# Performance work log

Hardware: AMD Instinct MI355X
Metric: run time of the kernel (lower is better)

The kernel has to match this reference:

```python
import jax, jax.numpy as jnp
import numpy as np

E = 2048   # embedding_size
H = 2048   # hidden_size
B = 512    # batch
OUT = 2    # output_size (coords)


def setup_inputs() -> dict:
    key = jax.random.key(0)
    ks = jax.random.split(key, 11)
    s = 0.02
    return {
        "embedding": jax.random.normal(ks[0], (B, E), dtype=jnp.float32),
        "max_seq_length": 256,
        "W_embed": jax.random.normal(ks[1], (H, E), dtype=jnp.float32) * s,
        "b_embed": jnp.zeros((H,), dtype=jnp.float32),
        "W_ih": jax.random.normal(ks[2], (4 * H, OUT), dtype=jnp.float32) * s,
        "b_ih": jnp.zeros((4 * H,), dtype=jnp.float32),
        "W_hh": jax.random.normal(ks[3], (4 * H, H), dtype=jnp.float32) * s,
        "b_hh": jnp.zeros((4 * H,), dtype=jnp.float32),
        "W_out": jax.random.normal(ks[4], (OUT, H), dtype=jnp.float32) * s,
        "b_out": jnp.zeros((OUT,), dtype=jnp.float32),
        "W_stop": jax.random.normal(ks[5], (1, H), dtype=jnp.float32) * s,
        "b_stop": jnp.zeros((1,), dtype=jnp.float32),
    }


def reference(embedding, max_seq_length, W_embed, b_embed, W_ih, b_ih,
              W_hh, b_hh, W_out, b_out, W_stop, b_stop):
    # h_0 from embedding head (num_layers == 1)
    h0 = embedding @ W_embed.T + b_embed          # (B, H)
    c0 = jnp.zeros_like(h0)
    x0 = jnp.zeros((embedding.shape[0], OUT), dtype=embedding.dtype)

    def step(carry, _):
        h, c, x = carry
        gates = x @ W_ih.T + b_ih + h @ W_hh.T + b_hh    # (B, 4H)
        i, f, g, o = jnp.split(gates, 4, axis=-1)         # torch gate order i,f,g,o
        c = jax.nn.sigmoid(f) * c + jax.nn.sigmoid(i) * jnp.tanh(g)
        h = jax.nn.sigmoid(o) * jnp.tanh(c)
        coord = h @ W_out.T + b_out                        # (B, 2)
        stop = jax.nn.sigmoid(h @ W_stop.T + b_stop)       # (B, 1)
        return (h, c, coord), (coord, stop)

    _, (coords, stops) = jax.lax.scan(step, (h0, c0, x0), xs=None,
                                      length=max_seq_length)
    outputs = jnp.transpose(coords, (1, 0, 2))     # (B, T, 2)
    stop_probs = jnp.transpose(stops, (1, 0, 2))   # (B, T, 1)
    return outputs, stop_probs
```

## Files before the change

kernel.cpp:

```cpp
#include <hip/hip_runtime.h>
#include <stdint.h>

#define E_DIM 2048
#define H_DIM 2048
#define B_DIM 512
#define T_DIM 256
#define G4H   8192

typedef unsigned short u16;
typedef __attribute__((ext_vector_type(8))) short bf16x8;
typedef __attribute__((ext_vector_type(4))) float f32x4;

__device__ inline u16 f2b(float f) {
  union { float f; uint32_t i; } v; v.f = f;
  uint32_t u = v.i;
  return (u16)((u + 0x7FFFu + ((u >> 16) & 1u)) >> 16);
}
__device__ inline float b2f(u16 u) {
  union { uint32_t i; float f; } v; v.i = ((uint32_t)u) << 16; return v.f;
}

__global__ __launch_bounds__(256) void convert_bf16(const float* __restrict__ s,
                                                    u16* __restrict__ d, int n4) {
  int i = blockIdx.x * 256 + threadIdx.x;
  if (i < n4) {
    float4 f = ((const float4*)s)[i];
    ushort4 o;
    o.x = f2b(f.x); o.y = f2b(f.y); o.z = f2b(f.z); o.w = f2b(f.w);
    ((ushort4*)d)[i] = o;
  }
}

__global__ __launch_bounds__(256) void build_wswz(const float* __restrict__ W,
                                                  u16* __restrict__ Wz) {
  int id = blockIdx.x * 256 + threadIdx.x;
  int lane = id & 63;
  int k32  = (id >> 6) & 63;
  int n16  = id >> 12;
  int np = n16 * 16 + (lane & 15);
  int k  = k32 * 32 + (lane >> 4) * 8;
  int g = np & 3, jrow = np >> 2;
  const float* src = W + (size_t)(g * H_DIM + jrow) * H_DIM + k;
  float4 f0 = *(const float4*)(src);
  float4 f1 = *(const float4*)(src + 4);
  ushort4 o0, o1;
  o0.x = f2b(f0.x); o0.y = f2b(f0.y); o0.z = f2b(f0.z); o0.w = f2b(f0.w);
  o1.x = f2b(f1.x); o1.y = f2b(f1.y); o1.z = f2b(f1.z); o1.w = f2b(f1.w);
  u16* dst = Wz + (size_t)id * 8;
  *(ushort4*)(dst) = o0;
  *(ushort4*)(dst + 4) = o1;
}

__global__ __launch_bounds__(256) void build_epi(const float* __restrict__ b_ih,
                                                 const float* __restrict__ b_hh,
                                                 const float* __restrict__ W_ih,
                                                 float* __restrict__ epi) {
  int np = blockIdx.x * 256 + threadIdx.x;
  int src = (np & 3) * H_DIM + (np >> 2);
  float4 e;
  e.x = b_ih[src] + b_hh[src];
  e.y = W_ih[src * 2];
  e.z = W_ih[src * 2 + 1];
  e.w = 0.f;
  ((float4*)epi)[np] = e;
}

#define BM 64
#define BN 128
#define BK 32
__global__ __launch_bounds__(256) void gemm_bt(const u16* __restrict__ A,
                                               const u16* __restrict__ Bm,
                                               float* __restrict__ C,
                                               int M, int N, int K) {
  __shared__ u16 sA[BM * BK];
  __shared__ u16 sB[BN * BK];
  const int t = threadIdx.x;
  const int bm0 = blockIdx.y * BM, bn0 = blockIdx.x * BN;
  const int wave = t >> 6, lane = t & 63;
  const int wm = (wave >> 1) * 32, wn = (wave & 1) * 64;
  const int r16 = lane & 15, quad = lane >> 4;

  f32x4 acc[2][4];
  const f32x4 z = {0.f, 0.f, 0.f, 0.f};
  for (int i = 0; i < 2; ++i)
    for (int j = 0; j < 4; ++j) acc[i][j] = z;

  const int arow = t >> 2, acg = t & 3;

  for (int k0 = 0; k0 < K; k0 += BK) {
    __syncthreads();
    *(uint4*)&sA[arow * BK + acg * 8] =
        *(const uint4*)&A[(size_t)(bm0 + arow) * K + k0 + acg * 8];
    for (int i = 0; i < 2; ++i) {
      int c = t + 256 * i;
      int row = c >> 2, cg = c & 3;
      *(uint4*)&sB[row * BK + cg * 8] =
          *(const uint4*)&Bm[(size_t)(bn0 + row) * K + k0 + cg * 8];
    }
    __syncthreads();
    bf16x8 af[2], bfr[4];
    for (int mt = 0; mt < 2; ++mt)
      af[mt] = *(const bf16x8*)&sA[(wm + mt * 16 + r16) * BK + quad * 8];
    for (int nt = 0; nt < 4; ++nt)
      bfr[nt] = *(const bf16x8*)&sB[(wn + nt * 16 + r16) * BK + quad * 8];
    for (int mt = 0; mt < 2; ++mt)
      for (int nt = 0; nt < 4; ++nt)
        acc[mt][nt] = __builtin_amdgcn_mfma_f32_16x16x32_bf16(af[mt], bfr[nt],
                                                              acc[mt][nt], 0, 0, 0);
  }
  for (int mt = 0; mt < 2; ++mt)
    for (int nt = 0; nt < 4; ++nt) {
      int row = bm0 + wm + mt * 16 + quad * 4;
      int col = bn0 + wn + nt * 16 + r16;
      for (int r = 0; r < 4; ++r)
        C[(size_t)(row + r) * N + col] = acc[mt][nt][r];
    }
}

__global__ __launch_bounds__(256) void init_state(const float* __restrict__ h0pre,
                                                  const float* __restrict__ b_embed,
                                                  u16* __restrict__ h,
                                                  float* __restrict__ c,
                                                  float* __restrict__ x) {
  int idx = blockIdx.x * 256 + threadIdx.x;
  int bg = idx >> 11, k = idx & (H_DIM - 1);
  float v = h0pre[idx] + b_embed[k];
  size_t chunk = (((size_t)(bg >> 4)) * 64 + (k >> 5)) * 64 + ((k >> 3) & 3) * 16 + (bg & 15);
  size_t pos = chunk * 8 + (k & 7);
  h[pos] = f2b(v);
  c[pos] = 0.f;
  if (idx < B_DIM * 2) x[idx] = 0.f;
}

__global__ __launch_bounds__(512) void gemm_lstm(const u16* __restrict__ hA,
                                                 const u16* __restrict__ Wz,
                                                 const float* __restrict__ epi,
                                                 const float* __restrict__ x,
                                                 float* __restrict__ c,
                                                 u16* __restrict__ h_out) {
  __shared__ char smem[33792];
  float* gt   = (float*)smem;
  float* comb = (float*)smem;

  const int bid = blockIdx.x;
  const int nt = (bid & 7) * 8 + ((bid >> 3) & 7);
  const int mt = bid >> 6;
  const int bm0 = mt * 128;

  const int t = threadIdx.x, wv = t >> 6, ln = t & 63;
  const int q = wv & 3, kh = wv >> 2;
  const int qm = q & 1, qn = q >> 1;
  const int r16 = ln & 15, quad = ln >> 4;

  const u16* pA[4];
  const u16* pB[4];
  for (int i = 0; i < 4; ++i) {
    pA[i] = hA + (size_t)((bm0 >> 4) + qm * 4 + i) * 32768 +
            (size_t)(kh * 32) * 512 + ln * 8;
    pB[i] = Wz + (size_t)(nt * 8 + qn * 4 + i) * 32768 +
            (size_t)(kh * 32) * 512 + ln * 8;
  }

  f32x4 acc[4][4];
  const f32x4 z = {0.f, 0.f, 0.f, 0.f};
  for (int i = 0; i < 4; ++i)
    for (int j = 0; j < 4; ++j) acc[i][j] = z;

  bf16x8 af[2][4], bf[2][4];
  for (int i = 0; i < 4; ++i) {
    af[0][i] = *(const bf16x8*)(pA[i]);
    bf[0][i] = *(const bf16x8*)(pB[i]);
  }

#pragma unroll 2
  for (int kk = 0; kk < 32; ++kk) {
    const int s = kk & 1;
    if (kk + 1 < 32) {
      const int sp = s ^ 1;
      for (int i = 0; i < 4; ++i) {
        af[sp][i] = *(const bf16x8*)(pA[i] + (size_t)(kk + 1) * 512);
        bf[sp][i] = *(const bf16x8*)(pB[i] + (size_t)(kk + 1) * 512);
      }
    }
    for (int mi = 0; mi < 4; ++mi)
      for (int ni = 0; ni < 4; ++ni)
        acc[mi][ni] = __builtin_amdgcn_mfma_f32_16x16x32_bf16(af[s][mi], bf[s][ni],
                                                              acc[mi][ni], 0, 0, 0);
  }

  for (int r = 0; r < 2; ++r) {
    __syncthreads();
    if (kh == 1 && qn == r) {
      float* dst = comb + qm * 4096;
      for (int mi = 0; mi < 4; ++mi)
        for (int ni = 0; ni < 4; ++ni)
          *(f32x4*)&dst[((mi * 4 + ni) * 64 + ln) * 4] = acc[mi][ni];
    }
    __syncthreads();
    if (kh == 0 && qn == r) {
      const float* src = comb + qm * 4096;
      for (int mi = 0; mi < 4; ++mi)
        for (int ni = 0; ni < 4; ++ni) {
          f32x4 p = *(const f32x4*)&src[((mi * 4 + ni) * 64 + ln) * 4];
          acc[mi][ni] += p;
        }
    }
  }

  for (int half = 0; half < 2; ++half) {
    __syncthreads();
    if (kh == 0 && qm == half) {
      for (int mi = 0; mi < 4; ++mi)
        for (int ni = 0; ni < 4; ++ni) {
          int row = mi * 16 + quad * 4;
          int col = qn * 64 + ni * 16 + r16;
          for (int r = 0; r < 4; ++r)
            gt[(row + r) * 132 + col] = acc[mi][ni][r];
        }
    }
    __syncthreads();
    if (kh == half) {
      const int lrow = q * 16 + r16;
      const int bg = bm0 + half * 64 + lrow;
      const float x0 = x[bg * 2 + 0], x1 = x[bg * 2 + 1];
      const size_t chunk = (((size_t)(bg >> 4)) * 64 + nt) * 64 + ln;
      float cv[8]; u16 hv[8];
      const float4* epi4 = (const float4*)epi;
      for (int j = 0; j < 8; ++j) {
        int col = quad * 32 + j * 4;
        float4 g4 = *(const float4*)&gt[lrow * 132 + col];
        float4 e0 = epi4[nt * 128 + col + 0];
        float4 e1 = epi4[nt * 128 + col + 1];
        float4 e2 = epi4[nt * 128 + col + 2];
        float4 e3 = epi4[nt * 128 + col + 3];
        float gi = g4.x + e0.x + x0 * e0.y + x1 * e0.z;
        float gf = g4.y + e1.x + x0 * e1.y + x1 * e1.z;
        float gg = g4.z + e2.x + x0 * e2.y + x1 * e2.z;
        float go = g4.w + e3.x + x0 * e3.y + x1 * e3.z;
        float si = 1.f / (1.f + __expf(-gi));
        float sf = 1.f / (1.f + __expf(-gf));
        float so = 1.f / (1.f + __expf(-go));
        float cn = sf * c[chunk * 8 + j] + si * tanhf(gg);
        cv[j] = cn;
        hv[j] = f2b(so * tanhf(cn));
      }
      *(float4*)&c[chunk * 8 + 0] = *(float4*)&cv[0];
      *(float4*)&c[chunk * 8 + 4] = *(float4*)&cv[4];
      *(ushort4*)&h_out[chunk * 8 + 0] = *(ushort4*)&hv[0];
      *(ushort4*)&h_out[chunk * 8 + 4] = *(ushort4*)&hv[4];
    }
  }
}

__global__ __launch_bounds__(256) void out_head(const u16* __restrict__ h,
                                                const float* __restrict__ W_out,
                                                const float* __restrict__ b_out,
                                                const float* __restrict__ W_stop,
                                                const float* __restrict__ b_stop,
                                                float* __restrict__ coords,
                                                float* __restrict__ stops,
                                                float* __restrict__ x, int t) {
  int bb = blockIdx.x;
  int tid = threadIdx.x;
  int k32 = tid >> 2, qd = tid & 3;
  size_t chunk = (((size_t)(bb >> 4)) * 64 + k32) * 64 + qd * 16 + (bb & 15);
  bf16x8 h8 = *(const bf16x8*)&h[chunk * 8];
  int kb = k32 * 32 + qd * 8;
  float s0 = 0.f, s1 = 0.f, s2 = 0.f;
  for (int j = 0; j < 8; ++j) {
    float hv = b2f((u16)h8[j]);
    s0 += hv * W_out[kb + j];
    s1 += hv * W_out[H_DIM + kb + j];
    s2 += hv * W_stop[kb + j];
  }
  for (int off = 32; off > 0; off >>= 1) {
    s0 += __shfl_down(s0, off);
    s1 += __shfl_down(s1, off);
    s2 += __shfl_down(s2, off);
  }
  __shared__ float red[4][3];
  int wave = tid >> 6, lane = tid & 63;
  if (lane == 0) { red[wave][0] = s0; red[wave][1] = s1; red[wave][2] = s2; }
  __syncthreads();
  if (tid == 0) {
    float c0 = red[0][0] + red[1][0] + red[2][0] + red[3][0] + b_out[0];
    float c1 = red[0][1] + red[1][1] + red[2][1] + red[3][1] + b_out[1];
    float sv = red[0][2] + red[1][2] + red[2][2] + red[3][2] + b_stop[0];
    float st = 1.f / (1.f + __expf(-sv));
    coords[((size_t)bb * T_DIM + t) * 2 + 0] = c0;
    coords[((size_t)bb * T_DIM + t) * 2 + 1] = c1;
    stops[(size_t)bb * T_DIM + t] = st;
    x[bb * 2 + 0] = c0;
    x[bb * 2 + 1] = c1;
  }
}

extern "C" void kernel_launch(void* const* d_in, const int* in_sizes, int n_in,
                              void* d_out, int out_size, void* d_ws, size_t ws_size,
                              hipStream_t stream) {
  const float* embedding = (const float*)d_in[0];
  const float* W_embed   = (const float*)d_in[2];
  const float* b_embed   = (const float*)d_in[3];
  const float* W_ih      = (const float*)d_in[4];
  const float* b_ih      = (const float*)d_in[5];
  const float* W_hh      = (const float*)d_in[6];
  const float* b_hh      = (const float*)d_in[7];
  const float* W_out     = (const float*)d_in[8];
  const float* b_out     = (const float*)d_in[9];
  const float* W_stop    = (const float*)d_in[10];
  const float* b_stop    = (const float*)d_in[11];

  float* coords = (float*)d_out;
  float* stops  = (float*)d_out + (size_t)B_DIM * T_DIM * 2;

  char* ws = (char*)d_ws;
  u16* W_z     = (u16*)ws;   ws += (size_t)G4H * H_DIM * 2;
  u16* W_emb_b = (u16*)ws;   ws += (size_t)H_DIM * E_DIM * 2;
  u16* emb_b   = (u16*)ws;   ws += (size_t)B_DIM * E_DIM * 2;
  float* h0pre = (float*)ws; ws += (size_t)B_DIM * H_DIM * 4;
  float* epi   = (float*)ws; ws += (size_t)G4H * 4 * 4;
  float* cbuf  = (float*)ws; ws += (size_t)B_DIM * H_DIM * 4;
  u16* hbuf0   = (u16*)ws;   ws += (size_t)B_DIM * H_DIM * 2;
  u16* hbuf1   = (u16*)ws;   ws += (size_t)B_DIM * H_DIM * 2;
  float* xbuf  = (float*)ws; ws += (size_t)B_DIM * 2 * 4;

  convert_bf16<<<(B_DIM * E_DIM / 4 + 255) / 256, 256, 0, stream>>>(embedding, emb_b, B_DIM * E_DIM / 4);
  convert_bf16<<<(H_DIM * E_DIM / 4 + 255) / 256, 256, 0, stream>>>(W_embed, W_emb_b, H_DIM * E_DIM / 4);
  build_wswz<<<(G4H * H_DIM / 8) / 256, 256, 0, stream>>>(W_hh, W_z);
  build_epi<<<G4H / 256, 256, 0, stream>>>(b_ih, b_hh, W_ih, epi);

  gemm_bt<<<dim3(H_DIM / BN, B_DIM / BM), 256, 0, stream>>>(emb_b, W_emb_b, h0pre,
                                                            B_DIM, H_DIM, E_DIM);
  init_state<<<(B_DIM * H_DIM) / 256, 256, 0, stream>>>(h0pre, b_embed, hbuf0, cbuf, xbuf);

  for (int t = 0; t < T_DIM; ++t) {
    u16* h_in  = (t & 1) ? hbuf1 : hbuf0;
    u16* h_out = (t & 1) ? hbuf0 : hbuf1;
    gemm_lstm<<<256, 512, 0, stream>>>(h_in, W_z, epi, xbuf, cbuf, h_out);
    out_head<<<B_DIM, 256, 0, stream>>>(h_out, W_out, b_out, W_stop, b_stop,
                                        coords, stops, xbuf, t);
  }
}
```

Measured before the change: 8.231 ms.

## Fold output projection into recurrent weights and fuse head into LSTM kernel

Since the next input x equals h·W_outᵀ+b_out, the input term W_ih·x is folded algebraically into an effective recurrent weight W_hh + W_ih·W_out and a bias correction, with a one-time correction term at t=0 where x is zero. This removes the per-step dependency on the coord output, so the out_head kernel is dropped and coords/stop logits are accumulated with atomics inside the LSTM epilogue. A final pass applies the stop sigmoid. This halves launches per step and removes a serial kernel, at the cost of atomic traffic and bf16 rounding of the combined weights, which changes numerics slightly.

```diff
diff --git a/kernel.cpp b/kernel.cpp
--- a/kernel.cpp
+++ b/kernel.cpp
@@ -31,7 +31,9 @@
   }
 }
 
-__global__ __launch_bounds__(256) void build_wswz(const float* __restrict__ W,
+__global__ __launch_bounds__(256) void build_weff(const float* __restrict__ W,
+                                                  const float* __restrict__ W_ih,
+                                                  const float* __restrict__ W_out,
                                                   u16* __restrict__ Wz) {
   int id = blockIdx.x * 256 + threadIdx.x;
   int lane = id & 63;
@@ -40,27 +42,31 @@
   int np = n16 * 16 + (lane & 15);
   int k  = k32 * 32 + (lane >> 4) * 8;
   int g = np & 3, jrow = np >> 2;
-  const float* src = W + (size_t)(g * H_DIM + jrow) * H_DIM + k;
-  float4 f0 = *(const float4*)(src);
-  float4 f1 = *(const float4*)(src + 4);
-  ushort4 o0, o1;
-  o0.x = f2b(f0.x); o0.y = f2b(f0.y); o0.z = f2b(f0.z); o0.w = f2b(f0.w);
-  o1.x = f2b(f1.x); o1.y = f2b(f1.y); o1.z = f2b(f1.z); o1.w = f2b(f1.w);
+  int src = g * H_DIM + jrow;
+  float wi0 = W_ih[src * 2 + 0], wi1 = W_ih[src * 2 + 1];
+  const float* sw = W + (size_t)src * H_DIM + k;
+  u16 out[8];
+  for (int j = 0; j < 8; ++j) {
+    float v = sw[j] + wi0 * W_out[k + j] + wi1 * W_out[H_DIM + k + j];
+    out[j] = f2b(v);
+  }
   u16* dst = Wz + (size_t)id * 8;
-  *(ushort4*)(dst) = o0;
-  *(ushort4*)(dst + 4) = o1;
+  *(ushort4*)(dst) = *(ushort4*)&out[0];
+  *(ushort4*)(dst + 4) = *(ushort4*)&out[4];
 }
 
 __global__ __launch_bounds__(256) void build_epi(const float* __restrict__ b_ih,
                                                  const float* __restrict__ b_hh,
                                                  const float* __restrict__ W_ih,
+                                                 const float* __restrict__ b_out,
                                                  float* __restrict__ epi) {
   int np = blockIdx.x * 256 + threadIdx.x;
   int src = (np & 3) * H_DIM + (np >> 2);
+  float wi0 = W_ih[src * 2 + 0], wi1 = W_ih[src * 2 + 1];
   float4 e;
-  e.x = b_ih[src] + b_hh[src];
-  e.y = W_ih[src * 2];
-  e.z = W_ih[src * 2 + 1];
+  e.x = b_ih[src] + b_hh[src] + b_out[0] * wi0 + b_out[1] * wi1;
+  e.y = wi0;
+  e.z = wi1;
   e.w = 0.f;
   ((float4*)epi)[np] = e;
 }
@@ -121,7 +127,7 @@
                                                   const float* __restrict__ b_embed,
                                                   u16* __restrict__ h,
                                                   float* __restrict__ c,
-                                                  float* __restrict__ x) {
+                                                  float* __restrict__ xzero) {
   int idx = blockIdx.x * 256 + threadIdx.x;
   int bg = idx >> 11, k = idx & (H_DIM - 1);
   float v = h0pre[idx] + b_embed[k];
@@ -129,7 +135,44 @@
   size_t pos = chunk * 8 + (k & 7);
   h[pos] = f2b(v);
   c[pos] = 0.f;
-  if (idx < B_DIM * 2) x[idx] = 0.f;
+  if (idx < B_DIM * 2) xzero[idx] = 0.f;
+}
+
+__global__ __launch_bounds__(64) void calc_xcorr(const float* __restrict__ h0pre,
+                                                 const float* __restrict__ b_embed,
+                                                 const float* __restrict__ W_out,
+                                                 const float* __restrict__ b_out,
+                                                 float* __restrict__ xc) {
+  int m = blockIdx.x, ln = threadIdx.x;
+  float s0 = 0.f, s1 = 0.f;
+  for (int k = ln; k < H_DIM; k += 64) {
+    float hv = h0pre[(size_t)m * H_DIM + k] + b_embed[k];
+    s0 += hv * W_out[k];
+    s1 += hv * W_out[H_DIM + k];
+  }
+  for (int off = 32; off > 0; off >>= 1) {
+    s0 += __shfl_down(s0, off);
+    s1 += __shfl_down(s1, off);
+  }
+  if (ln == 0) {
+    xc[m * 2 + 0] = -(s0 + b_out[0]);
+    xc[m * 2 + 1] = -(s1 + b_out[1]);
+  }
+}
+
+__global__ __launch_bounds__(256) void init_out(const float* __restrict__ b_out,
+                                                const float* __restrict__ b_stop,
+                                                float* __restrict__ coords,
+                                                float* __restrict__ stops) {
+  int i = blockIdx.x * 256 + threadIdx.x;
+  coords[i * 2 + 0] = b_out[0];
+  coords[i * 2 + 1] = b_out[1];
+  stops[i] = b_stop[0];
+}
+
+__global__ __launch_bounds__(256) void finalize_stops(float* __restrict__ stops) {
+  int i = blockIdx.x * 256 + threadIdx.x;
+  stops[i] = 1.f / (1.f + __expf(-stops[i]));
 }
 
 __global__ __launch_bounds__(512) void gemm_lstm(const u16* __restrict__ hA,
@@ -137,7 +180,12 @@
                                                  const float* __restrict__ epi,
                                                  const float* __restrict__ x,
                                                  float* __restrict__ c,
-                                                 u16* __restrict__ h_out) {
+                                                 u16* __restrict__ h_out,
+                                                 const float* __restrict__ W_out,
+                                                 const float* __restrict__ W_stop,
+                                                 float* __restrict__ coords,
+                                                 float* __restrict__ stops,
+                                                 int trow) {
   __shared__ char smem[33792];
   float* gt   = (float*)smem;
   float* comb = (float*)smem;
@@ -224,7 +272,9 @@
       const int bg = bm0 + half * 64 + lrow;
       const float x0 = x[bg * 2 + 0], x1 = x[bg * 2 + 1];
       const size_t chunk = (((size_t)(bg >> 4)) * 64 + nt) * 64 + ln;
+      const int hc0 = nt * 32 + quad * 8;
       float cv[8]; u16 hv[8];
+      float s0 = 0.f, s1 = 0.f, s2 = 0.f;
       const float4* epi4 = (const float4*)epi;
       for (int j = 0; j < 8; ++j) {
         int col = quad * 32 + j * 4;
@@ -242,56 +292,24 @@
         float so = 1.f / (1.f + __expf(-go));
         float cn = sf * c[chunk * 8 + j] + si * tanhf(gg);
         cv[j] = cn;
-        hv[j] = f2b(so * tanhf(cn));
+        float hf = so * tanhf(cn);
+        hv[j] = f2b(hf);
+        s0 += hf * W_out[hc0 + j];
+        s1 += hf * W_out[H_DIM + hc0 + j];
+        s2 += hf * W_stop[hc0 + j];
       }
       *(float4*)&c[chunk * 8 + 0] = *(float4*)&cv[0];
       *(float4*)&c[chunk * 8 + 4] = *(float4*)&cv[4];
       *(ushort4*)&h_out[chunk * 8 + 0] = *(ushort4*)&hv[0];
       *(ushort4*)&h_out[chunk * 8 + 4] = *(ushort4*)&hv[4];
-    }
-  }
-}
-
-__global__ __launch_bounds__(256) void out_head(const u16* __restrict__ h,
-                                                const float* __restrict__ W_out,
-                                                const float* __restrict__ b_out,
-                                                const float* __restrict__ W_stop,
-                                                const float* __restrict__ b_stop,
-                                                float* __restrict__ coords,
-                                                float* __restrict__ stops,
-                                                float* __restrict__ x, int t) {
-  int bb = blockIdx.x;
-  int tid = threadIdx.x;
-  int k32 = tid >> 2, qd = tid & 3;
-  size_t chunk = (((size_t)(bb >> 4)) * 64 + k32) * 64 + qd * 16 + (bb & 15);
-  bf16x8 h8 = *(const bf16x8*)&h[chunk * 8];
-  int kb = k32 * 32 + qd * 8;
-  float s0 = 0.f, s1 = 0.f, s2 = 0.f;
-  for (int j = 0; j < 8; ++j) {
-    float hv = b2f((u16)h8[j]);
-    s0 += hv * W_out[kb + j];
-    s1 += hv * W_out[H_DIM + kb + j];
-    s2 += hv * W_stop[kb + j];
-  }
-  for (int off = 32; off > 0; off >>= 1) {
-    s0 += __shfl_down(s0, off);
-    s1 += __shfl_down(s1, off);
-    s2 += __shfl_down(s2, off);
-  }
-  __shared__ float red[4][3];
-  int wave = tid >> 6, lane = tid & 63;
-  if (lane == 0) { red[wave][0] = s0; red[wave][1] = s1; red[wave][2] = s2; }
-  __syncthreads();
-  if (tid == 0) {
-    float c0 = red[0][0] + red[1][0] + red[2][0] + red[3][0] + b_out[0];
-    float c1 = red[0][1] + red[1][1] + red[2][1] + red[3][1] + b_out[1];
-    float sv = red[0][2] + red[1][2] + red[2][2] + red[3][2] + b_stop[0];
-    float st = 1.f / (1.f + __expf(-sv));
-    coords[((size_t)bb * T_DIM + t) * 2 + 0] = c0;
-    coords[((size_t)bb * T_DIM + t) * 2 + 1] = c1;
-    stops[(size_t)bb * T_DIM + t] = st;
-    x[bb * 2 + 0] = c0;
-    x[bb * 2 + 1] = c1;
+      s0 += __shfl_xor(s0, 16); s1 += __shfl_xor(s1, 16); s2 += __shfl_xor(s2, 16);
+      s0 += __shfl_xor(s0, 32); s1 += __shfl_xor(s1, 32); s2 += __shfl_xor(s2, 32);
+      if (quad == 0) {
+        atomicAdd(&coords[((size_t)bg * T_DIM + trow) * 2 + 0], s0);
+        atomicAdd(&coords[((size_t)bg * T_DIM + trow) * 2 + 1], s1);
+        atomicAdd(&stops[(size_t)bg * T_DIM + trow], s2);
+      }
+    }
   }
 }
 
@@ -322,22 +340,26 @@
   float* cbuf  = (float*)ws; ws += (size_t)B_DIM * H_DIM * 4;
   u16* hbuf0   = (u16*)ws;   ws += (size_t)B_DIM * H_DIM * 2;
   u16* hbuf1   = (u16*)ws;   ws += (size_t)B_DIM * H_DIM * 2;
-  float* xbuf  = (float*)ws; ws += (size_t)B_DIM * 2 * 4;
+  float* xcorr = (float*)ws; ws += (size_t)B_DIM * 2 * 4;
+  float* xzero = (float*)ws; ws += (size_t)B_DIM * 2 * 4;
 
   convert_bf16<<<(B_DIM * E_DIM / 4 + 255) / 256, 256, 0, stream>>>(embedding, emb_b, B_DIM * E_DIM / 4);
   convert_bf16<<<(H_DIM * E_DIM / 4 + 255) / 256, 256, 0, stream>>>(W_embed, W_emb_b, H_DIM * E_DIM / 4);
-  build_wswz<<<(G4H * H_DIM / 8) / 256, 256, 0, stream>>>(W_hh, W_z);
-  build_epi<<<G4H / 256, 256, 0, stream>>>(b_ih, b_hh, W_ih, epi);
+  build_weff<<<(G4H * H_DIM / 8) / 256, 256, 0, stream>>>(W_hh, W_ih, W_out, W_z);
+  build_epi<<<G4H / 256, 256, 0, stream>>>(b_ih, b_hh, W_ih, b_out, epi);
+  init_out<<<(B_DIM * T_DIM) / 256, 256, 0, stream>>>(b_out, b_stop, coords, stops);
 
   gemm_bt<<<dim3(H_DIM / BN, B_DIM / BM), 256, 0, stream>>>(emb_b, W_emb_b, h0pre,
                                                             B_DIM, H_DIM, E_DIM);
-  init_state<<<(B_DIM * H_DIM) / 256, 256, 0, stream>>>(h0pre, b_embed, hbuf0, cbuf, xbuf);
+  init_state<<<(B_DIM * H_DIM) / 256, 256, 0, stream>>>(h0pre, b_embed, hbuf0, cbuf, xzero);
+  calc_xcorr<<<B_DIM, 64, 0, stream>>>(h0pre, b_embed, W_out, b_out, xcorr);
 
   for (int t = 0; t < T_DIM; ++t) {
     u16* h_in  = (t & 1) ? hbuf1 : hbuf0;
     u16* h_out = (t & 1) ? hbuf0 : hbuf1;
-    gemm_lstm<<<256, 512, 0, stream>>>(h_in, W_z, epi, xbuf, cbuf, h_out);
-    out_head<<<B_DIM, 256, 0, stream>>>(h_out, W_out, b_out, W_stop, b_stop,
-                                        coords, stops, xbuf, t);
-  }
-}
+    const float* xv = (t == 0) ? xcorr : xzero;
+    gemm_lstm<<<256, 512, 0, stream>>>(h_in, W_z, epi, xv, cbuf, h_out,
+                                       W_out, W_stop, coords, stops, t);
+  }
+  finalize_stops<<<(B_DIM * T_DIM) / 256, 256, 0, stream>>>(stops);
+}
```

New measurement: 8.287 ms. No clear change (+0.7%).
